# Kernel optimization log

Hardware: AMD Instinct MI355X
Metric: run time of the kernel (lower is better)

## Reference

```python
import jax, jax.numpy as jnp
import numpy as np

N_AGENTS = 16
N_HEAD = 4      # Qatten heads (hardcoded in module)
EMBED = 64      # Qatten embed_dim (hardcoded)
N_KERNEL = 4    # SI weight kernels (hardcoded)
ACTION_DIM = N_AGENTS * N_AGENTS
B0, T = 256, 1024


def setup_inputs() -> dict:
    key = jax.random.key(0)
    ks = jax.random.split(key, 10)
    return {
        "agent_qs": jax.random.normal(ks[0], (B0, T, N_AGENTS), jnp.float32),
        "actions": jax.random.uniform(ks[1], (B0, T, ACTION_DIM), jnp.float32),
        "max_q_i": jax.random.normal(ks[2], (B0, T, N_AGENTS), jnp.float32),
        # Qatten_Weight params
        "selectors": jax.random.normal(ks[3], (N_HEAD, EMBED), jnp.float32),
        "keys": jax.random.normal(ks[4], (N_HEAD, EMBED), jnp.float32),
        "V": jax.random.normal(ks[5], (1,), jnp.float32),
        # DMAQ_SI_Weight params
        "si_keys": jax.random.normal(ks[6], (N_KERNEL,), jnp.float32),
        "si_agents": jax.random.normal(ks[7], (N_KERNEL, N_AGENTS), jnp.float32),
        "si_W": jax.random.normal(ks[8], (N_KERNEL, N_AGENTS, ACTION_DIM), jnp.float32) * (1.0 / np.sqrt(ACTION_DIM)),
        "si_b": jax.random.normal(ks[9], (N_KERNEL, N_AGENTS), jnp.float32) * 0.01,
    }


def reference(agent_qs, actions, max_q_i, selectors, keys, V, si_keys, si_agents, si_W, si_b):
    A = agent_qs.shape[-1]
    bs0 = agent_qs.shape[0]
    H, E = selectors.shape
    aq = agent_qs.reshape(-1, A)              # (B, A)
    mq = max_q_i.reshape(-1, A)               # (B, A)
    acts = actions.reshape(-1, si_W.shape[-1])  # (B, A*A)

    # --- Qatten_Weight: keys/selectors are per-head constant vectors broadcast
    # over batch & agents, so each head's logit is a single scalar dot product.
    logits = jnp.einsum('he,he->h', selectors, keys)        # (H,)
    scaled = logits / jnp.sqrt(jnp.asarray(E, jnp.float32))
    aw = jax.nn.softmax(jnp.broadcast_to(scaled[:, None], (H, A)), axis=-1)  # (H, A), uniform
    w_final = aw.sum(0) + 1e-10                             # (A,)
    attend_mag_regs = 0.001 * jnp.sum(logits ** 2)          # mean over constant == value
    head_entropies = -jnp.sum(jnp.log(aw + 1e-8) * aw, axis=-1)  # (H,)
    v = V[0] / A                                            # scalar, broadcast over (B, A)

    # --- mix agent qs
    aq2 = w_final * aq + v                                  # (B, A)
    mq2 = w_final * mq + v
    adv_q = jax.lax.stop_gradient(aq2 - mq2)                # .detach() in torch

    # --- DMAQ_SI_Weight (advantage weights)
    x_action = jax.nn.sigmoid(jnp.einsum('bd,kad->bka', acts, si_W) + si_b)  # (B, K, A)
    kern = (jnp.abs(si_keys)[:, None] + 1e-10) * jax.nn.sigmoid(si_agents)   # (K, A)
    adv_w = jnp.einsum('bka,ka->ba', x_action, kern)        # (B, A)

    adv_tot = jnp.sum(adv_q * (adv_w - 1.0), axis=1)        # (B,)
    v_tot = adv_tot.reshape(bs0, -1, 1)                     # (B0, T, 1)
    return (v_tot, attend_mag_regs, head_entropies)
```

## Files before the change

kernel.cpp:

```cpp
#include <hip/hip_runtime.h>
#include <hip/hip_bf16.h>


typedef __attribute__((ext_vector_type(8))) short short8;
typedef __attribute__((ext_vector_type(4))) short short4v;
typedef __attribute__((ext_vector_type(4))) float floatx4;

#define KDIM 252
#define ACT_K 256
#define NOUT 64
#define LDS_PITCH 264

__device__ __forceinline__ short f2bf(float f) {
  union { float f; unsigned u; } v; v.f = f;
  unsigned r = v.u + 0x7FFFu + ((v.u >> 16) & 1u);
  return (short)(r >> 16);
}

__device__ __forceinline__ float sigmoidf_fast(float x) {
  return 1.0f / (1.0f + __expf(-x));
}

__global__ __launch_bounds__(256) void mixer_main(
    const float* __restrict__ acts,
    const float* __restrict__ aq,
    const float* __restrict__ mq,
    const float* __restrict__ siW,
    const float* __restrict__ sib,
    const float* __restrict__ siKeys,
    const float* __restrict__ siAgents,
    float* __restrict__ out)
{
  __shared__ __align__(16) short ldsW[NOUT * LDS_PITCH];

  const int t = threadIdx.x;

  #pragma unroll
  for (int i = 0; i < 16; ++i) {
    int idx4 = i * 256 + t;
    int flat = idx4 * 4;
    int n = flat >> 8;
    int d = flat & 255;
    floatx4 w = *(const floatx4*)(siW + flat);
    short4v s;
    s[0] = f2bf(w.x); s[1] = f2bf(w.y); s[2] = f2bf(w.z); s[3] = f2bf(w.w);
    *(short4v*)(&ldsW[n * LDS_PITCH + d]) = s;
  }

  const int lane = t & 63;
  const int wv   = t >> 6;
  const int quad = lane >> 4;
  const int a    = lane & 15;
  const long rowBase = (long)blockIdx.x * 256 + (long)wv * 64;

  const float* aptr = acts + (rowBase + a) * ACT_K + quad * 8;
  const short* wbase = ldsW + a * LDS_PITCH + quad * 8;

  floatx4 acc[4][4];
  #pragma unroll
  for (int m = 0; m < 4; ++m)
    #pragma unroll
    for (int n = 0; n < 4; ++n)
      acc[m][n] = (floatx4){0.f, 0.f, 0.f, 0.f};

  __syncthreads();

  for (int ks = 0; ks < 8; ++ks) {
    short8 bf[4];
    #pragma unroll
    for (int n = 0; n < 4; ++n)
      bf[n] = *(const short8*)(wbase + n * 16 * LDS_PITCH + ks * 32);

    #pragma unroll
    for (int m = 0; m < 4; ++m) {
      const float* p = aptr + (long)m * 16 * ACT_K + ks * 32;
      floatx4 x0 = *(const floatx4*)(p);
      floatx4 x1 = *(const floatx4*)(p + 4);
      short8 af;
      af[0] = f2bf(x0.x); af[1] = f2bf(x0.y); af[2] = f2bf(x0.z); af[3] = f2bf(x0.w);
      af[4] = f2bf(x1.x); af[5] = f2bf(x1.y); af[6] = f2bf(x1.z); af[7] = f2bf(x1.w);
      #pragma unroll
      for (int n = 0; n < 4; ++n)
        acc[m][n] = __builtin_amdgcn_mfma_f32_16x16x32_bf16(af, bf[n], acc[m][n], 0, 0, 0);
    }
  }

  float kern[4], bias[4];
  #pragma unroll
  for (int k = 0; k < 4; ++k) {
    kern[k] = (fabsf(siKeys[k]) + 1e-10f) * sigmoidf_fast(siAgents[k * 16 + a]);
    bias[k] = sib[k * 16 + a];
  }

  #pragma unroll
  for (int m = 0; m < 4; ++m) {
    floatx4 res;
    #pragma unroll
    for (int r = 0; r < 4; ++r) {
      long b = rowBase + m * 16 + quad * 4 + r;
      float advw = 0.f;
      #pragma unroll
      for (int k = 0; k < 4; ++k) {
        float x = sigmoidf_fast(acc[m][k][r] + bias[k]);
        advw += x * kern[k];
      }
      float c = 0.25f * (aq[b * 16 + a] - mq[b * 16 + a]) * (advw - 1.0f);
      c += __shfl_xor(c, 8);
      c += __shfl_xor(c, 4);
      c += __shfl_xor(c, 2);
      c += __shfl_xor(c, 1);
      res[r] = c;
    }
    if (a == 0)
      *(floatx4*)(out + rowBase + m * 16 + quad * 4) = res;
  }
}

__global__ void mixer_scalars(const float* __restrict__ sel,
                              const float* __restrict__ keys,
                              float* __restrict__ out, int nrows)
{
  __shared__ float logits[4];
  const int t = threadIdx.x;
  float p = sel[t] * keys[t];
  #pragma unroll
  for (int m = 32; m; m >>= 1) p += __shfl_xor(p, m);
  if ((t & 63) == 0) logits[t >> 6] = p;
  __syncthreads();
  if (t == 0) {
    float s = 0.f;
    #pragma unroll
    for (int h = 0; h < 4; ++h) s += logits[h] * logits[h];
    out[nrows] = 0.001f * s;
  }
  if (t < 4)
    out[nrows + 1 + t] = -logf(0.0625f + 1e-8f);
}

extern "C" void kernel_launch(void* const* d_in, const int* in_sizes, int n_in,
                              void* d_out, int out_size, void* d_ws, size_t ws_size,
                              hipStream_t stream) {
  const float* agent_qs  = (const float*)d_in[0];
  const float* actions   = (const float*)d_in[1];
  const float* max_q_i   = (const float*)d_in[2];
  const float* selectors = (const float*)d_in[3];
  const float* keys      = (const float*)d_in[4];
  const float* si_keys   = (const float*)d_in[6];
  const float* si_agents = (const float*)d_in[7];
  const float* si_W      = (const float*)d_in[8];
  const float* si_b      = (const float*)d_in[9];
  float* out = (float*)d_out;

  const int nrows = in_sizes[0] / 16;
  const int blocks = nrows / 256;

  mixer_main<<<blocks, 256, 0, stream>>>(actions, agent_qs, max_q_i,
                                         si_W, si_b, si_keys, si_agents, out);
  mixer_scalars<<<1, 256, 0, stream>>>(selectors, keys, out, nrows);
}
```

Measured before the change: 404.7 us.

## Halve rows per wave, software-prefetch activations, fold scalar kernel into main

Each wave now handles 32 rows instead of 64, so blocks cover 128 rows and the grid doubles in size. The k-loop is fully unrolled and loads the next step's activation chunk while the current one is converted to bf16 and multiplied, hiding global-load latency. The separate scalar-output kernel is merged into the main kernel's first wave, removing one launch. The trade-off is that each block re-stages the full weight matrix into LDS for half as many rows, doubling that conversion work across the grid.

After: 399.9 us. No clear change (-1.2%).

```diff
diff --git a/kernel.cpp b/kernel.cpp
--- a/kernel.cpp
+++ b/kernel.cpp
@@ -6,10 +6,11 @@
 typedef __attribute__((ext_vector_type(4))) short short4v;
 typedef __attribute__((ext_vector_type(4))) float floatx4;
 
-#define KDIM 252
 #define ACT_K 256
 #define NOUT 64
 #define LDS_PITCH 264
+#define ROWS_PER_WAVE 32
+#define ROWS_PER_BLOCK 128
 
 __device__ __forceinline__ short f2bf(float f) {
   union { float f; unsigned u; } v; v.f = f;
@@ -29,7 +30,10 @@
     const float* __restrict__ sib,
     const float* __restrict__ siKeys,
     const float* __restrict__ siAgents,
-    float* __restrict__ out)
+    const float* __restrict__ sel,
+    const float* __restrict__ qkeys,
+    float* __restrict__ out,
+    int nrows)
 {
   __shared__ __align__(16) short ldsW[NOUT * LDS_PITCH];
 
@@ -51,38 +55,56 @@
   const int wv   = t >> 6;
   const int quad = lane >> 4;
   const int a    = lane & 15;
-  const long rowBase = (long)blockIdx.x * 256 + (long)wv * 64;
+  const long rowBase = (long)blockIdx.x * ROWS_PER_BLOCK + (long)wv * ROWS_PER_WAVE;
 
   const float* aptr = acts + (rowBase + a) * ACT_K + quad * 8;
   const short* wbase = ldsW + a * LDS_PITCH + quad * 8;
 
-  floatx4 acc[4][4];
+  floatx4 acc[2][4];
   #pragma unroll
-  for (int m = 0; m < 4; ++m)
+  for (int m = 0; m < 2; ++m)
     #pragma unroll
     for (int n = 0; n < 4; ++n)
       acc[m][n] = (floatx4){0.f, 0.f, 0.f, 0.f};
 
   __syncthreads();
 
+  floatx4 x[2][2];
+  #pragma unroll
+  for (int m = 0; m < 2; ++m) {
+    const float* p = aptr + (long)m * 16 * ACT_K;
+    x[m][0] = *(const floatx4*)(p);
+    x[m][1] = *(const floatx4*)(p + 4);
+  }
+
+  #pragma unroll
   for (int ks = 0; ks < 8; ++ks) {
     short8 bf[4];
     #pragma unroll
     for (int n = 0; n < 4; ++n)
       bf[n] = *(const short8*)(wbase + n * 16 * LDS_PITCH + ks * 32);
 
+    short8 af[2];
     #pragma unroll
-    for (int m = 0; m < 4; ++m) {
-      const float* p = aptr + (long)m * 16 * ACT_K + ks * 32;
-      floatx4 x0 = *(const floatx4*)(p);
-      floatx4 x1 = *(const floatx4*)(p + 4);
-      short8 af;
-      af[0] = f2bf(x0.x); af[1] = f2bf(x0.y); af[2] = f2bf(x0.z); af[3] = f2bf(x0.w);
-      af[4] = f2bf(x1.x); af[5] = f2bf(x1.y); af[6] = f2bf(x1.z); af[7] = f2bf(x1.w);
+    for (int m = 0; m < 2; ++m) {
+      af[m][0] = f2bf(x[m][0].x); af[m][1] = f2bf(x[m][0].y);
+      af[m][2] = f2bf(x[m][0].z); af[m][3] = f2bf(x[m][0].w);
+      af[m][4] = f2bf(x[m][1].x); af[m][5] = f2bf(x[m][1].y);
+      af[m][6] = f2bf(x[m][1].z); af[m][7] = f2bf(x[m][1].w);
+    }
+    if (ks < 7) {
+      #pragma unroll
+      for (int m = 0; m < 2; ++m) {
+        const float* p = aptr + (long)m * 16 * ACT_K + (ks + 1) * 32;
+        x[m][0] = *(const floatx4*)(p);
+        x[m][1] = *(const floatx4*)(p + 4);
+      }
+    }
+    #pragma unroll
+    for (int m = 0; m < 2; ++m)
       #pragma unroll
       for (int n = 0; n < 4; ++n)
-        acc[m][n] = __builtin_amdgcn_mfma_f32_16x16x32_bf16(af, bf[n], acc[m][n], 0, 0, 0);
-    }
+        acc[m][n] = __builtin_amdgcn_mfma_f32_16x16x32_bf16(af[m], bf[n], acc[m][n], 0, 0, 0);
   }
 
   float kern[4], bias[4];
@@ -93,7 +115,7 @@
   }
 
   #pragma unroll
-  for (int m = 0; m < 4; ++m) {
+  for (int m = 0; m < 2; ++m) {
     floatx4 res;
     #pragma unroll
     for (int r = 0; r < 4; ++r) {
@@ -101,8 +123,8 @@
       float advw = 0.f;
       #pragma unroll
       for (int k = 0; k < 4; ++k) {
-        float x = sigmoidf_fast(acc[m][k][r] + bias[k]);
-        advw += x * kern[k];
+        float xs = sigmoidf_fast(acc[m][k][r] + bias[k]);
+        advw += xs * kern[k];
       }
       float c = 0.25f * (aq[b * 16 + a] - mq[b * 16 + a]) * (advw - 1.0f);
       c += __shfl_xor(c, 8);
@@ -114,27 +136,19 @@
     if (a == 0)
       *(floatx4*)(out + rowBase + m * 16 + quad * 4) = res;
   }
-}
 
-__global__ void mixer_scalars(const float* __restrict__ sel,
-                              const float* __restrict__ keys,
-                              float* __restrict__ out, int nrows)
-{
-  __shared__ float logits[4];
-  const int t = threadIdx.x;
-  float p = sel[t] * keys[t];
-  #pragma unroll
-  for (int m = 32; m; m >>= 1) p += __shfl_xor(p, m);
-  if ((t & 63) == 0) logits[t >> 6] = p;
-  __syncthreads();
-  if (t == 0) {
+  if (blockIdx.x == 0 && wv == 0) {
     float s = 0.f;
     #pragma unroll
-    for (int h = 0; h < 4; ++h) s += logits[h] * logits[h];
-    out[nrows] = 0.001f * s;
+    for (int h = 0; h < 4; ++h) {
+      float p = sel[h * 64 + lane] * qkeys[h * 64 + lane];
+      #pragma unroll
+      for (int msk = 32; msk; msk >>= 1) p += __shfl_xor(p, msk);
+      s += p * p;
+    }
+    if (lane == 0) out[nrows] = 0.001f * s;
+    if (lane < 4)  out[nrows + 1 + lane] = -logf(0.0625f + 1e-8f);
   }
-  if (t < 4)
-    out[nrows + 1 + t] = -logf(0.0625f + 1e-8f);
 }
 
 extern "C" void kernel_launch(void* const* d_in, const int* in_sizes, int n_in,
@@ -152,9 +166,9 @@
   float* out = (float*)d_out;
 
   const int nrows = in_sizes[0] / 16;
-  const int blocks = nrows / 256;
+  const int blocks = nrows / ROWS_PER_BLOCK;
 
   mixer_main<<<blocks, 256, 0, stream>>>(actions, agent_qs, max_q_i,
-                                         si_W, si_b, si_keys, si_agents, out);
-  mixer_scalars<<<1, 256, 0, stream>>>(selectors, keys, out, nrows);
+                                         si_W, si_b, si_keys, si_agents,
+                                         selectors, keys, out, nrows);
 }
```
